# Kernel optimization log

Hardware: AMD Instinct MI355X
Metric: run time of the kernel (lower is better)

Reference implementation:

```python
import jax, jax.numpy as jnp
import numpy as np

L = 24          # num_layers
D_MODEL = 128   # hidden_size
EXPAND = 2
D_INNER = EXPAND * D_MODEL   # 256
D_STATE = 16
D_CONV = 4
DT_RANK = 8     # ceil(D_MODEL/16)
B, S = 2, 512
LN_EPS = 1e-5


def setup_inputs() -> dict:
    key = jax.random.key(0)
    ks = jax.random.split(key, 10)
    rn = lambda k, shape, sc=0.02: jax.random.normal(k, shape, jnp.float32) * sc
    s = jax.random.normal(ks[0], (B, S, D_MODEL), jnp.float32)
    z = jnp.zeros((B, S, S, D_MODEL), jnp.float32)
    # stacked per-layer Mamba params (mamba_ssm defaults: in_proj no bias, conv bias, out_proj no bias)
    in_proj_w = rn(ks[1], (L, 2 * D_INNER, D_MODEL))
    conv_w    = rn(ks[2], (L, D_INNER, D_CONV), 0.1)
    conv_b    = jnp.zeros((L, D_INNER), jnp.float32)
    x_proj_w  = rn(ks[3], (L, DT_RANK + 2 * D_STATE, D_INNER))
    dt_proj_w = rn(ks[4], (L, D_INNER, DT_RANK), 0.1)
    dt_proj_b = jnp.full((L, D_INNER), -4.6, jnp.float32)  # softplus(-4.6) ~ 0.01
    A_log = jnp.tile(jnp.log(jnp.arange(1, D_STATE + 1, dtype=jnp.float32))[None, None, :], (L, D_INNER, 1))
    D_skip = jnp.ones((L, D_INNER), jnp.float32)
    out_proj_w = rn(ks[5], (L, D_MODEL, D_INNER))
    ln_g = jnp.ones((L, D_MODEL), jnp.float32)
    ln_b = jnp.zeros((L, D_MODEL), jnp.float32)
    lin_w = rn(ks[6], (L, D_MODEL, D_MODEL))
    return dict(s=s, z=z, in_proj_w=in_proj_w, conv_w=conv_w, conv_b=conv_b,
                x_proj_w=x_proj_w, dt_proj_w=dt_proj_w, dt_proj_b=dt_proj_b,
                A_log=A_log, D_skip=D_skip, out_proj_w=out_proj_w,
                ln_g=ln_g, ln_b=ln_b, lin_w=lin_w)


def _mamba(u, Wi, cw, cb, Wx, Wdt, bdt, A_log, Dp, Wo):
    """mamba_ssm Mamba forward. u: [B,S,D_MODEL]."""
    Bb, Sl, _ = u.shape
    xz = jnp.einsum('bsd,ed->bse', u, Wi)            # [B,S,2*E]
    x, zg = jnp.split(xz, 2, axis=-1)                # each [B,S,E]
    # causal depthwise conv1d (padding=d_conv-1, truncated to seqlen)
    xp = jnp.pad(x, ((0, 0), (D_CONV - 1, 0), (0, 0)))
    x = sum(cw[:, k] * xp[:, k:k + Sl, :] for k in range(D_CONV)) + cb
    x = jax.nn.silu(x)
    proj = jnp.einsum('bse,pe->bsp', x, Wx)          # [B,S,dt_rank+2N]
    dt, Bm, Cm = jnp.split(proj, [DT_RANK, DT_RANK + D_STATE], axis=-1)
    dt = jax.nn.softplus(jnp.einsum('bsr,er->bse', dt, Wdt) + bdt)  # [B,S,E]
    A = -jnp.exp(A_log)                              # [E,N]
    dA = jnp.exp(dt[..., None] * A)                  # [B,S,E,N]
    dBx = (dt * x)[..., None] * Bm[:, :, None, :]    # [B,S,E,N]

    def step(h, inp):
        dA_t, dBx_t, C_t = inp
        h = dA_t * h + dBx_t                         # [B,E,N]
        y = jnp.einsum('ben,bn->be', h, C_t)
        return h, y

    h0 = jnp.zeros((Bb, D_INNER, D_STATE), u.dtype)
    _, ys = jax.lax.scan(step, h0, (dA.transpose(1, 0, 2, 3),
                                    dBx.transpose(1, 0, 2, 3),
                                    Cm.transpose(1, 0, 2)))
    y = ys.transpose(1, 0, 2) + x * Dp               # [B,S,E]
    y = y * jax.nn.silu(zg)
    return jnp.einsum('bse,de->bsd', y, Wo)          # [B,S,D_MODEL]


def _layernorm(x, g, b):
    mu = jnp.mean(x, axis=-1, keepdims=True)
    var = jnp.mean(jnp.square(x - mu), axis=-1, keepdims=True)
    return (x - mu) * jax.lax.rsqrt(var + LN_EPS) * g + b


def reference(s, z, in_proj_w, conv_w, conv_b, x_proj_w, dt_proj_w, dt_proj_b,
              A_log, D_skip, out_proj_w, ln_g, ln_b, lin_w):
    for i in range(L):
        m = _mamba(s, in_proj_w[i], conv_w[i], conv_b[i], x_proj_w[i],
                   dt_proj_w[i], dt_proj_b[i], A_log[i], D_skip[i], out_proj_w[i])
        m = _layernorm(m, ln_g[i], ln_b[i])
        m = jax.nn.relu(jnp.einsum('bsd,od->bso', m, lin_w[i]))
        s = s + m
        z = z + jnp.einsum('bsf,btf->bstf', s, s)
    return (s, z)
```

## Files before the change

### kernel.cpp

```cpp
#include <hip/hip_runtime.h>
#include <math.h>

#define LAYERS 24
#define DM 128
#define E 256
#define NST 16
#define RK 8
#define BATCH 2
#define SEQ 512
#define ROWS (BATCH*SEQ)
#define CS 8
#define NC (SEQ/CS)
#define SROWS (SEQ+3)
#define SPLANE (BATCH*SROWS*DM)

__device__ __forceinline__ float siluf_(float x) { return x / (1.0f + __expf(-x)); }
__device__ __forceinline__ float softplusf_(float x) {
    return (x > 20.0f) ? x : log1pf(__expf(x));
}

__global__ __launch_bounds__(256) void k_ab(
    const float* __restrict__ sP,
    const float* __restrict__ Wi,
    const float* __restrict__ cw,
    const float* __restrict__ cb,
    const float* __restrict__ Wx,
    const float* __restrict__ Wdt,
    const float* __restrict__ bdt,
    const float* __restrict__ Alog,
    float* __restrict__ xcg, float* __restrict__ dtg, float* __restrict__ szg,
    float* __restrict__ Bg, float* __restrict__ Cg,
    float* __restrict__ aprod, float* __restrict__ bsum)
{
    const int c = blockIdx.x & (NC - 1);
    const int b = blockIdx.x >> 6;
    const int tid = threadIdx.x;
    const int e = tid;
    const int t0 = c * CS;
    const float* __restrict__ srow = sP + ((size_t)b * SROWS + t0) * DM;

    __shared__ float xc_l[CS][E];
    __shared__ float prj[CS][RK + 2 * NST];

    float accx[11], accz[8];
    #pragma unroll
    for (int r = 0; r < 11; ++r) accx[r] = 0.0f;
    #pragma unroll
    for (int r = 0; r < 8; ++r) accz[r] = 0.0f;

    const float4* __restrict__ w0 = (const float4*)(Wi + (size_t)e * DM);
    const float4* __restrict__ w1 = (const float4*)(Wi + (size_t)(E + e) * DM);

    #pragma unroll 4
    for (int k4 = 0; k4 < 32; ++k4) {
        const float4 wa = w0[k4];
        const float4 wb = w1[k4];
        const float* sk = srow + k4 * 4;
        #pragma unroll
        for (int r = 0; r < 11; ++r) {
            const float4 sv = *(const float4*)(sk + r * DM);
            accx[r] = fmaf(wa.x, sv.x, fmaf(wa.y, sv.y,
                      fmaf(wa.z, sv.z, fmaf(wa.w, sv.w, accx[r]))));
            if (r >= 3) {
                accz[r - 3] = fmaf(wb.x, sv.x, fmaf(wb.y, sv.y,
                              fmaf(wb.z, sv.z, fmaf(wb.w, sv.w, accz[r - 3]))));
            }
        }
    }

    float xc[8], zg[8];
    {
        const float4 w4 = *(const float4*)(cw + e * 4);
        const float cbv = cb[e];
        #pragma unroll
        for (int r = 0; r < 8; ++r) {
            float v = cbv;
            v = fmaf(w4.x, accx[r], v);
            v = fmaf(w4.y, accx[r + 1], v);
            v = fmaf(w4.z, accx[r + 2], v);
            v = fmaf(w4.w, accx[r + 3], v);
            v = siluf_(v);
            xc[r] = v;
            xc_l[r][e] = v;
            zg[r] = siluf_(accz[r]);
        }
    }
    __syncthreads();

    #pragma unroll
    for (int pass = 0; pass < 2; ++pass) {
        const int p = (tid & 31) + pass * 32;
        const int row = tid >> 5;
        if (p < RK + 2 * NST) {
            const float4* __restrict__ wx4 = (const float4*)(Wx + (size_t)p * E);
            const float4* __restrict__ xr4 = (const float4*)(xc_l[row]);
            float s0 = 0.f, s1 = 0.f, s2 = 0.f, s3 = 0.f;
            #pragma unroll 8
            for (int qq = 0; qq < 64; ++qq) {
                const float4 w = wx4[qq];
                const float4 x = xr4[qq];
                s0 = fmaf(w.x, x.x, s0); s1 = fmaf(w.y, x.y, s1);
                s2 = fmaf(w.z, x.z, s2); s3 = fmaf(w.w, x.w, s3);
            }
            const float s = (s0 + s1) + (s2 + s3);
            prj[row][p] = s;
            const int t = t0 + row;
            if (p >= RK && p < RK + NST)
                Bg[((size_t)b * SEQ + t) * NST + (p - RK)] = s;
            else if (p >= RK + NST)
                Cg[((size_t)b * SEQ + t) * NST + (p - RK - NST)] = s;
        }
    }
    __syncthreads();

    float dt[8];
    {
        const float4 wd0 = *(const float4*)(Wdt + e * RK);
        const float4 wd1 = *(const float4*)(Wdt + e * RK + 4);
        const float bv = bdt[e];
        #pragma unroll
        for (int r = 0; r < 8; ++r) {
            float s = bv;
            s = fmaf(wd0.x, prj[r][0], s); s = fmaf(wd0.y, prj[r][1], s);
            s = fmaf(wd0.z, prj[r][2], s); s = fmaf(wd0.w, prj[r][3], s);
            s = fmaf(wd1.x, prj[r][4], s); s = fmaf(wd1.y, prj[r][5], s);
            s = fmaf(wd1.z, prj[r][6], s); s = fmaf(wd1.w, prj[r][7], s);
            dt[r] = softplusf_(s);
        }
    }

    float Av[NST];
    {
        const float4* al4 = (const float4*)(Alog + (size_t)e * NST);
        #pragma unroll
        for (int q = 0; q < 4; ++q) {
            const float4 v = al4[q];
            Av[q * 4 + 0] = -__expf(v.x);
            Av[q * 4 + 1] = -__expf(v.y);
            Av[q * 4 + 2] = -__expf(v.z);
            Av[q * 4 + 3] = -__expf(v.w);
        }
    }
    float ap[NST], bs[NST];
    #pragma unroll
    for (int n = 0; n < NST; ++n) { ap[n] = 1.0f; bs[n] = 0.0f; }
    #pragma unroll
    for (int r = 0; r < 8; ++r) {
        const float dtv = dt[r];
        const float dtx = dtv * xc[r];
        #pragma unroll
        for (int n = 0; n < NST; ++n) {
            const float dA = __expf(dtv * Av[n]);
            ap[n] *= dA;
            bs[n] = fmaf(dA, bs[n], dtx * prj[r][RK + n]);
        }
    }

    #pragma unroll
    for (int r = 0; r < 8; ++r) {
        const size_t rw = ((size_t)b * SEQ + t0 + r) * E + e;
        xcg[rw] = xc[r];
        dtg[rw] = dt[r];
        szg[rw] = zg[r];
    }
    const size_t base = ((size_t)(b * NC + c) * E + e) * NST;
    #pragma unroll
    for (int q = 0; q < 4; ++q) {
        *(float4*)(aprod + base + q * 4) =
            make_float4(ap[q*4], ap[q*4+1], ap[q*4+2], ap[q*4+3]);
        *(float4*)(bsum + base + q * 4) =
            make_float4(bs[q*4], bs[q*4+1], bs[q*4+2], bs[q*4+3]);
    }
}

__global__ __launch_bounds__(256) void k_prefix(const float* __restrict__ ap,
                                                const float* __restrict__ bs,
                                                float* __restrict__ h0)
{
    const int id = blockIdx.x * 256 + threadIdx.x;
    const int bb = id >> 12;
    const int en = id & 4095;
    float h = 0.0f;
    #pragma unroll
    for (int cc = 0; cc < NC; ++cc) {
        const size_t idx = (size_t)(bb * NC + cc) * (E * NST) + en;
        h0[idx] = h;
        h = fmaf(ap[idx], h, bs[idx]);
    }
}

__global__ __launch_bounds__(256) void k_cd(
    const float* __restrict__ h0, const float* __restrict__ xcg,
    const float* __restrict__ dtg, const float* __restrict__ szg,
    const float* __restrict__ Bg, const float* __restrict__ Cg,
    const float* __restrict__ Alog, const float* __restrict__ Dp,
    const float* __restrict__ Wo,
    const float* __restrict__ lng, const float* __restrict__ lnb,
    const float* __restrict__ Wl,
    const float* __restrict__ sPrev, float* __restrict__ sNext)
{
    const int c = blockIdx.x & (NC - 1);
    const int b = blockIdx.x >> 6;
    const int tid = threadIdx.x;
    const int e = tid;
    const int t0 = c * CS;

    __shared__ float BC[CS][2 * NST];
    __shared__ float yl[CS][E];
    __shared__ float ml[CS][DM];

    {
        const int r = tid >> 5, q = tid & 31;
        const size_t rw = ((size_t)b * SEQ + t0 + r) * NST;
        BC[r][q] = (q < NST) ? Bg[rw + q] : Cg[rw + (q - NST)];
    }

    float Av[NST], h[NST];
    {
        const float4* al4 = (const float4*)(Alog + (size_t)e * NST);
        const float4* h4 = (const float4*)(h0 + ((size_t)(b * NC + c) * E + e) * NST);
        #pragma unroll
        for (int q = 0; q < 4; ++q) {
            const float4 v = al4[q];
            Av[q * 4 + 0] = -__expf(v.x);
            Av[q * 4 + 1] = -__expf(v.y);
            Av[q * 4 + 2] = -__expf(v.z);
            Av[q * 4 + 3] = -__expf(v.w);
            const float4 hv = h4[q];
            h[q * 4 + 0] = hv.x; h[q * 4 + 1] = hv.y;
            h[q * 4 + 2] = hv.z; h[q * 4 + 3] = hv.w;
        }
    }
    const float Dv = Dp[e];
    __syncthreads();

    #pragma unroll
    for (int r = 0; r < 8; ++r) {
        const size_t rw = ((size_t)b * SEQ + t0 + r) * E + e;
        const float dtv = dtg[rw];
        const float xv = xcg[rw];
        const float dtx = dtv * xv;
        float y = 0.0f;
        #pragma unroll
        for (int n = 0; n < NST; ++n) {
            const float dA = __expf(dtv * Av[n]);
            h[n] = fmaf(dA, h[n], dtx * BC[r][n]);
            y = fmaf(h[n], BC[r][NST + n], y);
        }
        y = fmaf(xv, Dv, y) * szg[rw];
        yl[r][e] = y;
    }
    __syncthreads();

    const int row = tid >> 5, p5 = tid & 31;
    float mvals[4];
    #pragma unroll
    for (int pass = 0; pass < 4; ++pass) {
        const int d = p5 + pass * 32;
        const float4* __restrict__ wo4 = (const float4*)(Wo + (size_t)d * E);
        const float4* __restrict__ yr4 = (const float4*)(yl[row]);
        float s0 = 0.f, s1 = 0.f, s2 = 0.f, s3 = 0.f;
        #pragma unroll 8
        for (int qq = 0; qq < 64; ++qq) {
            const float4 w = wo4[qq];
            const float4 x = yr4[qq];
            s0 = fmaf(w.x, x.x, s0); s1 = fmaf(w.y, x.y, s1);
            s2 = fmaf(w.z, x.z, s2); s3 = fmaf(w.w, x.w, s3);
        }
        mvals[pass] = (s0 + s1) + (s2 + s3);
    }

    float s1 = mvals[0] + mvals[1] + mvals[2] + mvals[3];
    float s2 = mvals[0]*mvals[0] + mvals[1]*mvals[1]
             + mvals[2]*mvals[2] + mvals[3]*mvals[3];
    #pragma unroll
    for (int off = 16; off >= 1; off >>= 1) {
        s1 += __shfl_xor(s1, off);
        s2 += __shfl_xor(s2, off);
    }
    const float mean = s1 * (1.0f / 128.0f);
    const float var = s2 * (1.0f / 128.0f) - mean * mean;
    const float rstd = rsqrtf(var + 1e-5f);
    #pragma unroll
    for (int pass = 0; pass < 4; ++pass) {
        const int d = p5 + pass * 32;
        ml[row][d] = fmaf((mvals[pass] - mean) * rstd, lng[d], lnb[d]);
    }
    __syncthreads();

    #pragma unroll
    for (int pass = 0; pass < 4; ++pass) {
        const int d = p5 + pass * 32;
        const float4* __restrict__ wl4 = (const float4*)(Wl + (size_t)d * DM);
        const float4* __restrict__ lr4 = (const float4*)(ml[row]);
        float s0 = 0.f, s1_ = 0.f, s2_ = 0.f, s3 = 0.f;
        #pragma unroll 8
        for (int qq = 0; qq < 32; ++qq) {
            const float4 w = wl4[qq];
            const float4 x = lr4[qq];
            s0 = fmaf(w.x, x.x, s0); s1_ = fmaf(w.y, x.y, s1_);
            s2_ = fmaf(w.z, x.z, s2_); s3 = fmaf(w.w, x.w, s3);
        }
        const float v = fmaxf((s0 + s1_) + (s2_ + s3), 0.0f);
        const size_t off = ((size_t)b * SROWS + 3 + t0 + row) * DM + d;
        sNext[off] = sPrev[off] + v;
    }
}

__global__ __launch_bounds__(256) void k_z(const float* __restrict__ s_hist,
                                           float* __restrict__ z)
{
    const int bid = blockIdx.x;
    const int jt = bid & 63;
    const int it = (bid >> 6) & 31;
    const int fh = (bid >> 11) & 1;
    const int b  = bid >> 12;
    const int tid = threadIdx.x;
    const int q = tid & 15;
    const int u = tid >> 4;
    const int ig = u >> 2;
    const int jg = u & 3;
    const int i0 = it * 16 + ig * 4;
    const int j0 = jt * 8 + jg * 2;
    const int f0 = fh * 64 + q * 4;

    float4 acc[4][2];
    #pragma unroll
    for (int ii = 0; ii < 4; ++ii)
        #pragma unroll
        for (int jj = 0; jj < 2; ++jj)
            acc[ii][jj] = make_float4(0.f, 0.f, 0.f, 0.f);

    for (int l = 1; l <= LAYERS; ++l) {
        const float* sp = s_hist + (size_t)l * SPLANE + ((size_t)b * SROWS + 3) * DM;
        const float4 sj0 = *(const float4*)(sp + (size_t)(j0 + 0) * DM + f0);
        const float4 sj1 = *(const float4*)(sp + (size_t)(j0 + 1) * DM + f0);
        #pragma unroll
        for (int ii = 0; ii < 4; ++ii) {
            const float4 si = *(const float4*)(sp + (size_t)(i0 + ii) * DM + f0);
            acc[ii][0].x = fmaf(si.x, sj0.x, acc[ii][0].x);
            acc[ii][0].y = fmaf(si.y, sj0.y, acc[ii][0].y);
            acc[ii][0].z = fmaf(si.z, sj0.z, acc[ii][0].z);
            acc[ii][0].w = fmaf(si.w, sj0.w, acc[ii][0].w);
            acc[ii][1].x = fmaf(si.x, sj1.x, acc[ii][1].x);
            acc[ii][1].y = fmaf(si.y, sj1.y, acc[ii][1].y);
            acc[ii][1].z = fmaf(si.z, sj1.z, acc[ii][1].z);
            acc[ii][1].w = fmaf(si.w, sj1.w, acc[ii][1].w);
        }
    }
    #pragma unroll
    for (int ii = 0; ii < 4; ++ii)
        #pragma unroll
        for (int jj = 0; jj < 2; ++jj) {
            const size_t off = (((size_t)b * SEQ + i0 + ii) * SEQ + (j0 + jj)) * DM + f0;
            *(float4*)(z + off) = acc[ii][jj];
        }
}

extern "C" void kernel_launch(void* const* d_in, const int* in_sizes, int n_in,
                              void* d_out, int out_size, void* d_ws, size_t ws_size,
                              hipStream_t stream)
{
    const float* in_s = (const float*)d_in[0];
    const float* W_in = (const float*)d_in[2];
    const float* cw   = (const float*)d_in[3];
    const float* cb   = (const float*)d_in[4];
    const float* Wx   = (const float*)d_in[5];
    const float* Wdt  = (const float*)d_in[6];
    const float* bdt  = (const float*)d_in[7];
    const float* Alog = (const float*)d_in[8];
    const float* Dp   = (const float*)d_in[9];
    const float* Wo   = (const float*)d_in[10];
    const float* lng  = (const float*)d_in[11];
    const float* lnb  = (const float*)d_in[12];
    const float* Wl   = (const float*)d_in[13];
    float* out = (float*)d_out;

    float* ws = (float*)d_ws;
    float* s_hist = ws;
    float* xcg   = s_hist + (size_t)25 * SPLANE;
    float* dtg   = xcg + (size_t)ROWS * E;
    float* szg   = dtg + (size_t)ROWS * E;
    float* Bg    = szg + (size_t)ROWS * E;
    float* Cg    = Bg + (size_t)ROWS * NST;
    float* aprod = Cg + (size_t)ROWS * NST;
    float* bsum  = aprod + (size_t)BATCH * NC * E * NST;
    float* h0    = bsum + (size_t)BATCH * NC * E * NST;

    hipMemsetAsync(s_hist, 0, (size_t)25 * SPLANE * sizeof(float), stream);
    for (int b = 0; b < BATCH; ++b)
        hipMemcpyAsync(s_hist + ((size_t)b * SROWS + 3) * DM,
                       in_s + (size_t)b * SEQ * DM,
                       (size_t)SEQ * DM * sizeof(float),
                       hipMemcpyDeviceToDevice, stream);

    for (int l = 0; l < LAYERS; ++l) {
        const float* sP = s_hist + (size_t)l * SPLANE;
        float* sN = s_hist + (size_t)(l + 1) * SPLANE;
        k_ab<<<BATCH * NC, 256, 0, stream>>>(
            sP, W_in + (size_t)l * 512 * DM, cw + (size_t)l * E * 4, cb + (size_t)l * E,
            Wx + (size_t)l * (RK + 2 * NST) * E, Wdt + (size_t)l * E * RK,
            bdt + (size_t)l * E, Alog + (size_t)l * E * NST,
            xcg, dtg, szg, Bg, Cg, aprod, bsum);
        k_prefix<<<32, 256, 0, stream>>>(aprod, bsum, h0);
        k_cd<<<BATCH * NC, 256, 0, stream>>>(
            h0, xcg, dtg, szg, Bg, Cg, Alog + (size_t)l * E * NST, Dp + (size_t)l * E,
            Wo + (size_t)l * DM * E, lng + (size_t)l * DM, lnb + (size_t)l * DM,
            Wl + (size_t)l * DM * DM, sP, sN);
    }

    for (int b = 0; b < BATCH; ++b)
        hipMemcpyAsync(out + (size_t)b * SEQ * DM,
                       s_hist + (size_t)LAYERS * SPLANE + ((size_t)b * SROWS + 3) * DM,
                       (size_t)SEQ * DM * sizeof(float),
                       hipMemcpyDeviceToDevice, stream);
    k_z<<<BATCH * 2 * 32 * 64, 256, 0, stream>>>(s_hist, out + (size_t)ROWS * DM);
}
```

Baseline: 2.482 ms.

## Fuse all layers into one cooperative persistent kernel and retile z outer-product

```diff
diff --git a/kernel.cpp b/kernel.cpp
--- a/kernel.cpp
+++ b/kernel.cpp
@@ -1,5 +1,8 @@
 #include <hip/hip_runtime.h>
+#include <hip/hip_cooperative_groups.h>
 #include <math.h>
+
+namespace cg = cooperative_groups;
 
 #define LAYERS 24
 #define DM 128
@@ -9,7 +12,7 @@
 #define BATCH 2
 #define SEQ 512
 #define ROWS (BATCH*SEQ)
-#define CS 8
+#define CS 4
 #define NC (SEQ/CS)
 #define SROWS (SEQ+3)
 #define SPLANE (BATCH*SROWS*DM)
@@ -19,291 +22,241 @@
     return (x > 20.0f) ? x : log1pf(__expf(x));
 }
 
-__global__ __launch_bounds__(256) void k_ab(
-    const float* __restrict__ sP,
-    const float* __restrict__ Wi,
-    const float* __restrict__ cw,
-    const float* __restrict__ cb,
-    const float* __restrict__ Wx,
-    const float* __restrict__ Wdt,
-    const float* __restrict__ bdt,
-    const float* __restrict__ Alog,
-    float* __restrict__ xcg, float* __restrict__ dtg, float* __restrict__ szg,
-    float* __restrict__ Bg, float* __restrict__ Cg,
-    float* __restrict__ aprod, float* __restrict__ bsum)
+__global__ __launch_bounds__(256) void k_chain(
+    const float* __restrict__ Wi, const float* __restrict__ cw,
+    const float* __restrict__ cb, const float* __restrict__ Wx,
+    const float* __restrict__ Wdt, const float* __restrict__ bdt,
+    const float* __restrict__ Alog, const float* __restrict__ Dp,
+    const float* __restrict__ Wo, const float* __restrict__ lng,
+    const float* __restrict__ lnb, const float* __restrict__ Wl,
+    float* __restrict__ s_hist, float* __restrict__ aprod,
+    float* __restrict__ bsum, float* __restrict__ h0g)
 {
-    const int c = blockIdx.x & (NC - 1);
-    const int b = blockIdx.x >> 6;
+    cg::grid_group grid = cg::this_grid();
+    const int bid = blockIdx.x;
     const int tid = threadIdx.x;
+    const int b = bid >> 7;
+    const int c = bid & (NC - 1);
+    const int t0 = c * CS;
     const int e = tid;
-    const int t0 = c * CS;
-    const float* __restrict__ srow = sP + ((size_t)b * SROWS + t0) * DM;
-
+
+    __shared__ float s_s[CS + 3][DM];
     __shared__ float xc_l[CS][E];
     __shared__ float prj[CS][RK + 2 * NST];
-
-    float accx[11], accz[8];
-    #pragma unroll
-    for (int r = 0; r < 11; ++r) accx[r] = 0.0f;
-    #pragma unroll
-    for (int r = 0; r < 8; ++r) accz[r] = 0.0f;
-
-    const float4* __restrict__ w0 = (const float4*)(Wi + (size_t)e * DM);
-    const float4* __restrict__ w1 = (const float4*)(Wi + (size_t)(E + e) * DM);
-
-    #pragma unroll 4
-    for (int k4 = 0; k4 < 32; ++k4) {
-        const float4 wa = w0[k4];
-        const float4 wb = w1[k4];
-        const float* sk = srow + k4 * 4;
-        #pragma unroll
-        for (int r = 0; r < 11; ++r) {
-            const float4 sv = *(const float4*)(sk + r * DM);
-            accx[r] = fmaf(wa.x, sv.x, fmaf(wa.y, sv.y,
-                      fmaf(wa.z, sv.z, fmaf(wa.w, sv.w, accx[r]))));
-            if (r >= 3) {
-                accz[r - 3] = fmaf(wb.x, sv.x, fmaf(wb.y, sv.y,
-                              fmaf(wb.z, sv.z, fmaf(wb.w, sv.w, accz[r - 3]))));
-            }
-        }
-    }
-
-    float xc[8], zg[8];
-    {
-        const float4 w4 = *(const float4*)(cw + e * 4);
-        const float cbv = cb[e];
-        #pragma unroll
-        for (int r = 0; r < 8; ++r) {
-            float v = cbv;
-            v = fmaf(w4.x, accx[r], v);
-            v = fmaf(w4.y, accx[r + 1], v);
-            v = fmaf(w4.z, accx[r + 2], v);
-            v = fmaf(w4.w, accx[r + 3], v);
-            v = siluf_(v);
-            xc[r] = v;
-            xc_l[r][e] = v;
-            zg[r] = siluf_(accz[r]);
-        }
-    }
-    __syncthreads();
-
-    #pragma unroll
-    for (int pass = 0; pass < 2; ++pass) {
-        const int p = (tid & 31) + pass * 32;
-        const int row = tid >> 5;
-        if (p < RK + 2 * NST) {
-            const float4* __restrict__ wx4 = (const float4*)(Wx + (size_t)p * E);
-            const float4* __restrict__ xr4 = (const float4*)(xc_l[row]);
-            float s0 = 0.f, s1 = 0.f, s2 = 0.f, s3 = 0.f;
-            #pragma unroll 8
-            for (int qq = 0; qq < 64; ++qq) {
-                const float4 w = wx4[qq];
-                const float4 x = xr4[qq];
-                s0 = fmaf(w.x, x.x, s0); s1 = fmaf(w.y, x.y, s1);
-                s2 = fmaf(w.z, x.z, s2); s3 = fmaf(w.w, x.w, s3);
-            }
-            const float s = (s0 + s1) + (s2 + s3);
-            prj[row][p] = s;
-            const int t = t0 + row;
-            if (p >= RK && p < RK + NST)
-                Bg[((size_t)b * SEQ + t) * NST + (p - RK)] = s;
-            else if (p >= RK + NST)
-                Cg[((size_t)b * SEQ + t) * NST + (p - RK - NST)] = s;
-        }
-    }
-    __syncthreads();
-
-    float dt[8];
-    {
-        const float4 wd0 = *(const float4*)(Wdt + e * RK);
-        const float4 wd1 = *(const float4*)(Wdt + e * RK + 4);
-        const float bv = bdt[e];
-        #pragma unroll
-        for (int r = 0; r < 8; ++r) {
-            float s = bv;
-            s = fmaf(wd0.x, prj[r][0], s); s = fmaf(wd0.y, prj[r][1], s);
-            s = fmaf(wd0.z, prj[r][2], s); s = fmaf(wd0.w, prj[r][3], s);
-            s = fmaf(wd1.x, prj[r][4], s); s = fmaf(wd1.y, prj[r][5], s);
-            s = fmaf(wd1.z, prj[r][6], s); s = fmaf(wd1.w, prj[r][7], s);
-            dt[r] = softplusf_(s);
-        }
-    }
-
-    float Av[NST];
-    {
-        const float4* al4 = (const float4*)(Alog + (size_t)e * NST);
-        #pragma unroll
-        for (int q = 0; q < 4; ++q) {
-            const float4 v = al4[q];
-            Av[q * 4 + 0] = -__expf(v.x);
-            Av[q * 4 + 1] = -__expf(v.y);
-            Av[q * 4 + 2] = -__expf(v.z);
-            Av[q * 4 + 3] = -__expf(v.w);
-        }
-    }
-    float ap[NST], bs[NST];
-    #pragma unroll
-    for (int n = 0; n < NST; ++n) { ap[n] = 1.0f; bs[n] = 0.0f; }
-    #pragma unroll
-    for (int r = 0; r < 8; ++r) {
-        const float dtv = dt[r];
-        const float dtx = dtv * xc[r];
-        #pragma unroll
-        for (int n = 0; n < NST; ++n) {
-            const float dA = __expf(dtv * Av[n]);
-            ap[n] *= dA;
-            bs[n] = fmaf(dA, bs[n], dtx * prj[r][RK + n]);
-        }
-    }
-
-    #pragma unroll
-    for (int r = 0; r < 8; ++r) {
-        const size_t rw = ((size_t)b * SEQ + t0 + r) * E + e;
-        xcg[rw] = xc[r];
-        dtg[rw] = dt[r];
-        szg[rw] = zg[r];
-    }
-    const size_t base = ((size_t)(b * NC + c) * E + e) * NST;
-    #pragma unroll
-    for (int q = 0; q < 4; ++q) {
-        *(float4*)(aprod + base + q * 4) =
-            make_float4(ap[q*4], ap[q*4+1], ap[q*4+2], ap[q*4+3]);
-        *(float4*)(bsum + base + q * 4) =
-            make_float4(bs[q*4], bs[q*4+1], bs[q*4+2], bs[q*4+3]);
-    }
-}
-
-__global__ __launch_bounds__(256) void k_prefix(const float* __restrict__ ap,
-                                                const float* __restrict__ bs,
-                                                float* __restrict__ h0)
-{
-    const int id = blockIdx.x * 256 + threadIdx.x;
-    const int bb = id >> 12;
-    const int en = id & 4095;
-    float h = 0.0f;
-    #pragma unroll
-    for (int cc = 0; cc < NC; ++cc) {
-        const size_t idx = (size_t)(bb * NC + cc) * (E * NST) + en;
-        h0[idx] = h;
-        h = fmaf(ap[idx], h, bs[idx]);
-    }
-}
-
-__global__ __launch_bounds__(256) void k_cd(
-    const float* __restrict__ h0, const float* __restrict__ xcg,
-    const float* __restrict__ dtg, const float* __restrict__ szg,
-    const float* __restrict__ Bg, const float* __restrict__ Cg,
-    const float* __restrict__ Alog, const float* __restrict__ Dp,
-    const float* __restrict__ Wo,
-    const float* __restrict__ lng, const float* __restrict__ lnb,
-    const float* __restrict__ Wl,
-    const float* __restrict__ sPrev, float* __restrict__ sNext)
-{
-    const int c = blockIdx.x & (NC - 1);
-    const int b = blockIdx.x >> 6;
-    const int tid = threadIdx.x;
-    const int e = tid;
-    const int t0 = c * CS;
-
-    __shared__ float BC[CS][2 * NST];
     __shared__ float yl[CS][E];
     __shared__ float ml[CS][DM];
 
-    {
-        const int r = tid >> 5, q = tid & 31;
-        const size_t rw = ((size_t)b * SEQ + t0 + r) * NST;
-        BC[r][q] = (q < NST) ? Bg[rw + q] : Cg[rw + (q - NST)];
-    }
-
-    float Av[NST], h[NST];
-    {
-        const float4* al4 = (const float4*)(Alog + (size_t)e * NST);
-        const float4* h4 = (const float4*)(h0 + ((size_t)(b * NC + c) * E + e) * NST);
-        #pragma unroll
-        for (int q = 0; q < 4; ++q) {
-            const float4 v = al4[q];
-            Av[q * 4 + 0] = -__expf(v.x);
-            Av[q * 4 + 1] = -__expf(v.y);
-            Av[q * 4 + 2] = -__expf(v.z);
-            Av[q * 4 + 3] = -__expf(v.w);
-            const float4 hv = h4[q];
-            h[q * 4 + 0] = hv.x; h[q * 4 + 1] = hv.y;
-            h[q * 4 + 2] = hv.z; h[q * 4 + 3] = hv.w;
-        }
-    }
-    const float Dv = Dp[e];
-    __syncthreads();
-
-    #pragma unroll
-    for (int r = 0; r < 8; ++r) {
-        const size_t rw = ((size_t)b * SEQ + t0 + r) * E + e;
-        const float dtv = dtg[rw];
-        const float xv = xcg[rw];
-        const float dtx = dtv * xv;
-        float y = 0.0f;
-        #pragma unroll
-        for (int n = 0; n < NST; ++n) {
-            const float dA = __expf(dtv * Av[n]);
-            h[n] = fmaf(dA, h[n], dtx * BC[r][n]);
-            y = fmaf(h[n], BC[r][NST + n], y);
-        }
-        y = fmaf(xv, Dv, y) * szg[rw];
-        yl[r][e] = y;
-    }
-    __syncthreads();
-
-    const int row = tid >> 5, p5 = tid & 31;
-    float mvals[4];
-    #pragma unroll
-    for (int pass = 0; pass < 4; ++pass) {
-        const int d = p5 + pass * 32;
-        const float4* __restrict__ wo4 = (const float4*)(Wo + (size_t)d * E);
-        const float4* __restrict__ yr4 = (const float4*)(yl[row]);
-        float s0 = 0.f, s1 = 0.f, s2 = 0.f, s3 = 0.f;
-        #pragma unroll 8
-        for (int qq = 0; qq < 64; ++qq) {
-            const float4 w = wo4[qq];
-            const float4 x = yr4[qq];
-            s0 = fmaf(w.x, x.x, s0); s1 = fmaf(w.y, x.y, s1);
-            s2 = fmaf(w.z, x.z, s2); s3 = fmaf(w.w, x.w, s3);
-        }
-        mvals[pass] = (s0 + s1) + (s2 + s3);
-    }
-
-    float s1 = mvals[0] + mvals[1] + mvals[2] + mvals[3];
-    float s2 = mvals[0]*mvals[0] + mvals[1]*mvals[1]
-             + mvals[2]*mvals[2] + mvals[3]*mvals[3];
-    #pragma unroll
-    for (int off = 16; off >= 1; off >>= 1) {
-        s1 += __shfl_xor(s1, off);
-        s2 += __shfl_xor(s2, off);
-    }
-    const float mean = s1 * (1.0f / 128.0f);
-    const float var = s2 * (1.0f / 128.0f) - mean * mean;
-    const float rstd = rsqrtf(var + 1e-5f);
-    #pragma unroll
-    for (int pass = 0; pass < 4; ++pass) {
-        const int d = p5 + pass * 32;
-        ml[row][d] = fmaf((mvals[pass] - mean) * rstd, lng[d], lnb[d]);
-    }
-    __syncthreads();
-
-    #pragma unroll
-    for (int pass = 0; pass < 4; ++pass) {
-        const int d = p5 + pass * 32;
-        const float4* __restrict__ wl4 = (const float4*)(Wl + (size_t)d * DM);
-        const float4* __restrict__ lr4 = (const float4*)(ml[row]);
-        float s0 = 0.f, s1_ = 0.f, s2_ = 0.f, s3 = 0.f;
-        #pragma unroll 8
-        for (int qq = 0; qq < 32; ++qq) {
-            const float4 w = wl4[qq];
-            const float4 x = lr4[qq];
-            s0 = fmaf(w.x, x.x, s0); s1_ = fmaf(w.y, x.y, s1_);
-            s2_ = fmaf(w.z, x.z, s2_); s3 = fmaf(w.w, x.w, s3);
-        }
-        const float v = fmaxf((s0 + s1_) + (s2_ + s3), 0.0f);
-        const size_t off = ((size_t)b * SROWS + 3 + t0 + row) * DM + d;
-        sNext[off] = sPrev[off] + v;
+    for (int l = 0; l < LAYERS; ++l) {
+        const float* __restrict__ sPl = s_hist + (size_t)l * SPLANE;
+        {
+            const float4* sPc = (const float4*)(sPl + ((size_t)b * SROWS + t0) * DM);
+            if (tid < (CS + 3) * DM / 4) ((float4*)s_s)[tid] = sPc[tid];
+        }
+        __syncthreads();
+
+        float accx[CS + 3], accz[CS];
+        #pragma unroll
+        for (int r = 0; r < CS + 3; ++r) accx[r] = 0.f;
+        #pragma unroll
+        for (int r = 0; r < CS; ++r) accz[r] = 0.f;
+        {
+            const float4* __restrict__ wx4 = (const float4*)(Wi + ((size_t)l * 2 * E + e) * DM);
+            const float4* __restrict__ wz4 = (const float4*)(Wi + ((size_t)l * 2 * E + E + e) * DM);
+            #pragma unroll 4
+            for (int k4 = 0; k4 < DM / 4; ++k4) {
+                const float4 wa = wx4[k4];
+                const float4 wb = wz4[k4];
+                #pragma unroll
+                for (int r = 0; r < CS + 3; ++r) {
+                    const float4 sv = *(const float4*)&s_s[r][k4 * 4];
+                    accx[r] = fmaf(wa.x, sv.x, fmaf(wa.y, sv.y,
+                              fmaf(wa.z, sv.z, fmaf(wa.w, sv.w, accx[r]))));
+                    if (r >= 3) {
+                        float t = accz[r - 3];
+                        t = fmaf(wb.x, sv.x, fmaf(wb.y, sv.y,
+                            fmaf(wb.z, sv.z, fmaf(wb.w, sv.w, t))));
+                        accz[r - 3] = t;
+                    }
+                }
+            }
+        }
+        float xc[CS], zg[CS];
+        {
+            const float4 w4 = *(const float4*)(cw + ((size_t)l * E + e) * 4);
+            const float cbv = cb[(size_t)l * E + e];
+            #pragma unroll
+            for (int r = 0; r < CS; ++r) {
+                float v = cbv;
+                v = fmaf(w4.x, accx[r], v);
+                v = fmaf(w4.y, accx[r + 1], v);
+                v = fmaf(w4.z, accx[r + 2], v);
+                v = fmaf(w4.w, accx[r + 3], v);
+                v = siluf_(v);
+                xc[r] = v;
+                xc_l[r][e] = v;
+                zg[r] = siluf_(accz[r]);
+            }
+        }
+        __syncthreads();
+        {
+            const int row = tid >> 6, p = tid & 63;
+            if (p < RK + 2 * NST) {
+                const float4* __restrict__ wp = (const float4*)(Wx + ((size_t)l * 40 + p) * E);
+                const float4* __restrict__ xr = (const float4*)xc_l[row];
+                float a0 = 0.f, a1 = 0.f, a2 = 0.f, a3 = 0.f;
+                #pragma unroll 8
+                for (int q4 = 0; q4 < E / 4; ++q4) {
+                    const float4 w = wp[q4];
+                    const float4 x = xr[q4];
+                    a0 = fmaf(w.x, x.x, a0); a1 = fmaf(w.y, x.y, a1);
+                    a2 = fmaf(w.z, x.z, a2); a3 = fmaf(w.w, x.w, a3);
+                }
+                prj[row][p] = (a0 + a1) + (a2 + a3);
+            }
+        }
+        __syncthreads();
+        float dt[CS];
+        {
+            const float4 wd0 = *(const float4*)(Wdt + ((size_t)l * E + e) * RK);
+            const float4 wd1 = *(const float4*)(Wdt + ((size_t)l * E + e) * RK + 4);
+            const float bv = bdt[(size_t)l * E + e];
+            #pragma unroll
+            for (int r = 0; r < CS; ++r) {
+                float s = bv;
+                s = fmaf(wd0.x, prj[r][0], s); s = fmaf(wd0.y, prj[r][1], s);
+                s = fmaf(wd0.z, prj[r][2], s); s = fmaf(wd0.w, prj[r][3], s);
+                s = fmaf(wd1.x, prj[r][4], s); s = fmaf(wd1.y, prj[r][5], s);
+                s = fmaf(wd1.z, prj[r][6], s); s = fmaf(wd1.w, prj[r][7], s);
+                dt[r] = softplusf_(s);
+            }
+        }
+        float Av[NST];
+        {
+            const float4* al4 = (const float4*)(Alog + ((size_t)l * E + e) * NST);
+            #pragma unroll
+            for (int q = 0; q < 4; ++q) {
+                const float4 v = al4[q];
+                Av[q * 4 + 0] = -__expf(v.x); Av[q * 4 + 1] = -__expf(v.y);
+                Av[q * 4 + 2] = -__expf(v.z); Av[q * 4 + 3] = -__expf(v.w);
+            }
+        }
+        {
+            float ap[NST], bs[NST];
+            #pragma unroll
+            for (int n = 0; n < NST; ++n) { ap[n] = 1.f; bs[n] = 0.f; }
+            #pragma unroll
+            for (int r = 0; r < CS; ++r) {
+                const float dtx = dt[r] * xc[r];
+                #pragma unroll
+                for (int n = 0; n < NST; ++n) {
+                    const float dA = __expf(dt[r] * Av[n]);
+                    ap[n] *= dA;
+                    bs[n] = fmaf(dA, bs[n], dtx * prj[r][RK + n]);
+                }
+            }
+            const size_t base = ((size_t)bid * E + e) * NST;
+            #pragma unroll
+            for (int q = 0; q < 4; ++q) {
+                *(float4*)(aprod + base + q * 4) =
+                    make_float4(ap[q*4], ap[q*4+1], ap[q*4+2], ap[q*4+3]);
+                *(float4*)(bsum + base + q * 4) =
+                    make_float4(bs[q*4], bs[q*4+1], bs[q*4+2], bs[q*4+3]);
+            }
+        }
+        grid.sync();
+        if (bid < BATCH * E * NST / 256) {
+            const int gi = bid * 256 + tid;
+            const int bb = gi >> 12;
+            const int en = gi & (E * NST - 1);
+            float h = 0.f;
+            #pragma unroll 8
+            for (int cc = 0; cc < NC; ++cc) {
+                const size_t idx = (size_t)(bb * NC + cc) * (E * NST) + en;
+                h0g[idx] = h;
+                h = fmaf(aprod[idx], h, bsum[idx]);
+            }
+        }
+        grid.sync();
+        {
+            float h[NST];
+            const float4* h4 = (const float4*)(h0g + ((size_t)bid * E + e) * NST);
+            #pragma unroll
+            for (int q = 0; q < 4; ++q) {
+                const float4 v = h4[q];
+                h[q*4+0] = v.x; h[q*4+1] = v.y; h[q*4+2] = v.z; h[q*4+3] = v.w;
+            }
+            const float Dv = Dp[(size_t)l * E + e];
+            #pragma unroll
+            for (int r = 0; r < CS; ++r) {
+                const float dtx = dt[r] * xc[r];
+                float y = 0.f;
+                #pragma unroll
+                for (int n = 0; n < NST; ++n) {
+                    const float dA = __expf(dt[r] * Av[n]);
+                    h[n] = fmaf(dA, h[n], dtx * prj[r][RK + n]);
+                    y = fmaf(h[n], prj[r][RK + NST + n], y);
+                }
+                yl[r][e] = fmaf(xc[r], Dv, y) * zg[r];
+            }
+        }
+        __syncthreads();
+        const int row = tid >> 6, d0 = tid & 63;
+        {
+            const float* Wol = Wo + (size_t)l * DM * E;
+            const float4* __restrict__ w0 = (const float4*)(Wol + (size_t)d0 * E);
+            const float4* __restrict__ w1 = (const float4*)(Wol + (size_t)(d0 + 64) * E);
+            const float4* __restrict__ yr = (const float4*)yl[row];
+            float a0=0.f,a1=0.f,a2=0.f,a3=0.f,b0=0.f,b1=0.f,b2=0.f,b3=0.f;
+            #pragma unroll 8
+            for (int q4 = 0; q4 < E / 4; ++q4) {
+                const float4 yv = yr[q4];
+                const float4 wv0 = w0[q4], wv1 = w1[q4];
+                a0 = fmaf(wv0.x, yv.x, a0); a1 = fmaf(wv0.y, yv.y, a1);
+                a2 = fmaf(wv0.z, yv.z, a2); a3 = fmaf(wv0.w, yv.w, a3);
+                b0 = fmaf(wv1.x, yv.x, b0); b1 = fmaf(wv1.y, yv.y, b1);
+                b2 = fmaf(wv1.z, yv.z, b2); b3 = fmaf(wv1.w, yv.w, b3);
+            }
+            const float mv0 = (a0 + a1) + (a2 + a3);
+            const float mv1 = (b0 + b1) + (b2 + b3);
+            float s1 = mv0 + mv1;
+            float s2 = mv0 * mv0 + mv1 * mv1;
+            #pragma unroll
+            for (int off = 32; off >= 1; off >>= 1) {
+                s1 += __shfl_xor(s1, off);
+                s2 += __shfl_xor(s2, off);
+            }
+            const float mean = s1 * (1.0f / 128.0f);
+            const float var = s2 * (1.0f / 128.0f) - mean * mean;
+            const float rstd = rsqrtf(var + 1e-5f);
+            ml[row][d0]      = fmaf((mv0 - mean) * rstd, lng[(size_t)l * DM + d0],
+                                    lnb[(size_t)l * DM + d0]);
+            ml[row][d0 + 64] = fmaf((mv1 - mean) * rstd, lng[(size_t)l * DM + d0 + 64],
+                                    lnb[(size_t)l * DM + d0 + 64]);
+        }
+        __syncthreads();
+        {
+            const float* Wll = Wl + (size_t)l * DM * DM;
+            const float4* __restrict__ w0 = (const float4*)(Wll + (size_t)d0 * DM);
+            const float4* __restrict__ w1 = (const float4*)(Wll + (size_t)(d0 + 64) * DM);
+            const float4* __restrict__ mr = (const float4*)ml[row];
+            float a0=0.f,a1=0.f,a2=0.f,a3=0.f,b0=0.f,b1=0.f,b2=0.f,b3=0.f;
+            #pragma unroll 8
+            for (int q4 = 0; q4 < DM / 4; ++q4) {
+                const float4 xv = mr[q4];
+                const float4 wv0 = w0[q4], wv1 = w1[q4];
+                a0 = fmaf(wv0.x, xv.x, a0); a1 = fmaf(wv0.y, xv.y, a1);
+                a2 = fmaf(wv0.z, xv.z, a2); a3 = fmaf(wv0.w, xv.w, a3);
+                b0 = fmaf(wv1.x, xv.x, b0); b1 = fmaf(wv1.y, xv.y, b1);
+                b2 = fmaf(wv1.z, xv.z, b2); b3 = fmaf(wv1.w, xv.w, b3);
+            }
+            const float v0 = fmaxf((a0 + a1) + (a2 + a3), 0.0f);
+            const float v1 = fmaxf((b0 + b1) + (b2 + b3), 0.0f);
+            float* __restrict__ sN = s_hist + (size_t)(l + 1) * SPLANE;
+            const size_t ro = ((size_t)b * SROWS + 3 + t0 + row) * DM;
+            sN[ro + d0]      = s_s[3 + row][d0] + v0;
+            sN[ro + d0 + 64] = s_s[3 + row][d0 + 64] + v1;
+        }
+        grid.sync();
     }
 }
 
@@ -311,50 +264,61 @@
                                            float* __restrict__ z)
 {
     const int bid = blockIdx.x;
-    const int jt = bid & 63;
-    const int it = (bid >> 6) & 31;
-    const int fh = (bid >> 11) & 1;
-    const int b  = bid >> 12;
+    const int jt = bid & 31;
+    const int it = (bid >> 5) & 31;
+    const int b  = bid >> 10;
     const int tid = threadIdx.x;
-    const int q = tid & 15;
-    const int u = tid >> 4;
+    const int q = tid & 31;
+    const int u = tid >> 5;
     const int ig = u >> 2;
     const int jg = u & 3;
-    const int i0 = it * 16 + ig * 4;
-    const int j0 = jt * 8 + jg * 2;
-    const int f0 = fh * 64 + q * 4;
-
-    float4 acc[4][2];
+    const int i0 = it * 16, j0 = jt * 16;
+
+    __shared__ float4 si[16][32];
+    __shared__ float4 sj[16][32];
+
+    float4 acc[8][4];
     #pragma unroll
-    for (int ii = 0; ii < 4; ++ii)
-        #pragma unroll
-        for (int jj = 0; jj < 2; ++jj)
+    for (int ii = 0; ii < 8; ++ii)
+        #pragma unroll
+        for (int jj = 0; jj < 4; ++jj)
             acc[ii][jj] = make_float4(0.f, 0.f, 0.f, 0.f);
 
     for (int l = 1; l <= LAYERS; ++l) {
         const float* sp = s_hist + (size_t)l * SPLANE + ((size_t)b * SROWS + 3) * DM;
-        const float4 sj0 = *(const float4*)(sp + (size_t)(j0 + 0) * DM + f0);
-        const float4 sj1 = *(const float4*)(sp + (size_t)(j0 + 1) * DM + f0);
-        #pragma unroll
-        for (int ii = 0; ii < 4; ++ii) {
-            const float4 si = *(const float4*)(sp + (size_t)(i0 + ii) * DM + f0);
-            acc[ii][0].x = fmaf(si.x, sj0.x, acc[ii][0].x);
-            acc[ii][0].y = fmaf(si.y, sj0.y, acc[ii][0].y);
-            acc[ii][0].z = fmaf(si.z, sj0.z, acc[ii][0].z);
-            acc[ii][0].w = fmaf(si.w, sj0.w, acc[ii][0].w);
-            acc[ii][1].x = fmaf(si.x, sj1.x, acc[ii][1].x);
-            acc[ii][1].y = fmaf(si.y, sj1.y, acc[ii][1].y);
-            acc[ii][1].z = fmaf(si.z, sj1.z, acc[ii][1].z);
-            acc[ii][1].w = fmaf(si.w, sj1.w, acc[ii][1].w);
+        __syncthreads();
+        #pragma unroll
+        for (int k = 0; k < 2; ++k) {
+            const int idx = k * 256 + tid;
+            const int rr = idx >> 5, c4 = idx & 31;
+            si[rr][c4] = *(const float4*)(sp + (size_t)(i0 + rr) * DM + c4 * 4);
+            sj[rr][c4] = *(const float4*)(sp + (size_t)(j0 + rr) * DM + c4 * 4);
+        }
+        __syncthreads();
+        float4 bv[4];
+        #pragma unroll
+        for (int jj = 0; jj < 4; ++jj) bv[jj] = sj[jg * 4 + jj][q];
+        #pragma unroll
+        for (int ii = 0; ii < 8; ++ii) {
+            const float4 av = si[ig * 8 + ii][q];
+            #pragma unroll
+            for (int jj = 0; jj < 4; ++jj) {
+                acc[ii][jj].x = fmaf(av.x, bv[jj].x, acc[ii][jj].x);
+                acc[ii][jj].y = fmaf(av.y, bv[jj].y, acc[ii][jj].y);
+                acc[ii][jj].z = fmaf(av.z, bv[jj].z, acc[ii][jj].z);
+                acc[ii][jj].w = fmaf(av.w, bv[jj].w, acc[ii][jj].w);
+            }
         }
     }
     #pragma unroll
-    for (int ii = 0; ii < 4; ++ii)
-        #pragma unroll
-        for (int jj = 0; jj < 2; ++jj) {
-            const size_t off = (((size_t)b * SEQ + i0 + ii) * SEQ + (j0 + jj)) * DM + f0;
-            *(float4*)(z + off) = acc[ii][jj];
-        }
+    for (int ii = 0; ii < 8; ++ii) {
+        const int i = i0 + ig * 8 + ii;
+        #pragma unroll
+        for (int jj = 0; jj < 4; ++jj) {
+            const int j = j0 + jg * 4 + jj;
+            *(float4*)(z + (((size_t)b * SEQ + i) * SEQ + j) * DM + q * 4) = acc[ii][jj];
+        }
+    }
 }
 
 extern "C" void kernel_launch(void* const* d_in, const int* in_sizes, int n_in,
@@ -378,14 +342,9 @@
 
     float* ws = (float*)d_ws;
     float* s_hist = ws;
-    float* xcg   = s_hist + (size_t)25 * SPLANE;
-    float* dtg   = xcg + (size_t)ROWS * E;
-    float* szg   = dtg + (size_t)ROWS * E;
-    float* Bg    = szg + (size_t)ROWS * E;
-    float* Cg    = Bg + (size_t)ROWS * NST;
-    float* aprod = Cg + (size_t)ROWS * NST;
-    float* bsum  = aprod + (size_t)BATCH * NC * E * NST;
-    float* h0    = bsum + (size_t)BATCH * NC * E * NST;
+    float* aprod  = s_hist + (size_t)25 * SPLANE;
+    float* bsum   = aprod + (size_t)BATCH * NC * E * NST;
+    float* h0g    = bsum + (size_t)BATCH * NC * E * NST;
 
     hipMemsetAsync(s_hist, 0, (size_t)25 * SPLANE * sizeof(float), stream);
     for (int b = 0; b < BATCH; ++b)
@@ -394,25 +353,19 @@
                        (size_t)SEQ * DM * sizeof(float),
                        hipMemcpyDeviceToDevice, stream);
 
-    for (int l = 0; l < LAYERS; ++l) {
-        const float* sP = s_hist + (size_t)l * SPLANE;
-        float* sN = s_hist + (size_t)(l + 1) * SPLANE;
-        k_ab<<<BATCH * NC, 256, 0, stream>>>(
-            sP, W_in + (size_t)l * 512 * DM, cw + (size_t)l * E * 4, cb + (size_t)l * E,
-            Wx + (size_t)l * (RK + 2 * NST) * E, Wdt + (size_t)l * E * RK,
-            bdt + (size_t)l * E, Alog + (size_t)l * E * NST,
-            xcg, dtg, szg, Bg, Cg, aprod, bsum);
-        k_prefix<<<32, 256, 0, stream>>>(aprod, bsum, h0);
-        k_cd<<<BATCH * NC, 256, 0, stream>>>(
-            h0, xcg, dtg, szg, Bg, Cg, Alog + (size_t)l * E * NST, Dp + (size_t)l * E,
-            Wo + (size_t)l * DM * E, lng + (size_t)l * DM, lnb + (size_t)l * DM,
-            Wl + (size_t)l * DM * DM, sP, sN);
-    }
+    void* args[] = {
+        (void*)&W_in, (void*)&cw, (void*)&cb, (void*)&Wx,
+        (void*)&Wdt, (void*)&bdt, (void*)&Alog, (void*)&Dp,
+        (void*)&Wo, (void*)&lng, (void*)&lnb, (void*)&Wl,
+        (void*)&s_hist, (void*)&aprod, (void*)&bsum, (void*)&h0g
+    };
+    hipLaunchCooperativeKernel(reinterpret_cast<void*>(k_chain),
+                               dim3(BATCH * NC), dim3(256), args, 0, stream);
 
     for (int b = 0; b < BATCH; ++b)
         hipMemcpyAsync(out + (size_t)b * SEQ * DM,
                        s_hist + (size_t)LAYERS * SPLANE + ((size_t)b * SROWS + 3) * DM,
                        (size_t)SEQ * DM * sizeof(float),
                        hipMemcpyDeviceToDevice, stream);
-    k_z<<<BATCH * 2 * 32 * 64, 256, 0, stream>>>(s_hist, out + (size_t)ROWS * DM);
+    k_z<<<BATCH * 32 * 32, 256, 0, stream>>>(s_hist, out + (size_t)ROWS * DM);
 }
```

Result: slower. 3.605 ms (+45.2%).
